# Kernel optimization log

Measured on AMD Instinct MI355X. Metric: run time of the kernel, lower is better.

Reference implementation:

```python
import jax, jax.numpy as jnp
import numpy as np

N = 1_048_576   # number of input points
C = 64          # feature channels
GRID = 128      # voxels per spatial dim
BATCH = 4


def setup_inputs() -> dict:
    key = jax.random.key(0)
    k1, k2, k3 = jax.random.split(key, 3)
    # coords layout per scn: [x, y, z, batch_idx]
    xyz = jax.random.randint(k1, (N, 3), 0, GRID, dtype=jnp.int64)
    b = jax.random.randint(k2, (N, 1), 0, BATCH, dtype=jnp.int64)
    coords = jnp.concatenate([xyz, b], axis=1)
    features = jax.random.normal(k3, (N, C), dtype=jnp.float32)
    spatial_size = jnp.array([GRID, GRID, GRID], dtype=jnp.int64)
    return {"coords": coords, "features": features,
            "spatial_size": spatial_size, "batch_size": BATCH}


def reference(coords, features, spatial_size, batch_size):
    # Hash each (batch, x, y, z) coordinate to a unique linear voxel id,
    # then scatter-SUM (scn mode=3) features of duplicate coordinates.
    n = coords.shape[0]
    # row-major strides over spatial dims: [S1*S2, S2, 1]
    strides = jnp.concatenate([
        jnp.cumprod(spatial_size[::-1])[::-1][1:], jnp.ones((1,), jnp.int64)])
    vol = jnp.prod(spatial_size)
    lin = coords[:, -1] * vol + coords[:, :-1] @ strides  # [N] voxel ids

    # Unique active sites (padded to fixed size N for jit) + inverse map.
    uniq_ids, inv = jnp.unique(lin, size=n, fill_value=-1, return_inverse=True)
    inv = inv.reshape(n)

    # Scatter-reduce features into active sites (mode 3 = sum duplicates).
    sparse_features = jax.ops.segment_sum(features, inv, num_segments=n)
    return uniq_ids, sparse_features
```

## Files before the change

### kernel.cpp

```cpp
#include <hip/hip_runtime.h>

constexpr int GRID_D = 128;
constexpr int BATCHN = 4;
constexpr int C = 64;
constexpr int VOL = GRID_D * GRID_D * GRID_D;
constexpr int V = BATCHN * VOL;
constexpr int W = V / 32;
constexpr int SCAN_BS = 1024;
constexpr int SCAN_NB = W / SCAN_BS;

typedef float floatx4 __attribute__((ext_vector_type(4)));


__global__ void zero_ws(uint4* __restrict__ p, int count) {
    int i = blockIdx.x * blockDim.x + threadIdx.x;
    if (i < count) p[i] = uint4{0u, 0u, 0u, 0u};
}

__global__ void mark_bits(const int* __restrict__ coords, unsigned* __restrict__ bm,
                          unsigned* __restrict__ lin, int n) {
    int i = blockIdx.x * blockDim.x + threadIdx.x;
    if (i >= n) return;
    int4 co = reinterpret_cast<const int4*>(coords)[i];
    unsigned l = (unsigned)(co.w * VOL + co.x * (GRID_D * GRID_D) + co.y * GRID_D + co.z);
    lin[i] = l;
    atomicOr(&bm[l >> 5], 1u << (l & 31));
}

__global__ void scan1(const unsigned* __restrict__ bm, unsigned* __restrict__ wp,
                      unsigned* __restrict__ bs) {
    int idx = blockIdx.x * SCAN_BS + threadIdx.x;
    unsigned pc = __popc(bm[idx]);
    unsigned v = pc;
    #pragma unroll
    for (int d = 1; d < 64; d <<= 1) {
        unsigned t = __shfl_up(v, d, 64);
        if ((threadIdx.x & 63) >= d) v += t;
    }
    __shared__ unsigned wsum[16];
    int wid = threadIdx.x >> 6;
    int lane = threadIdx.x & 63;
    if (lane == 63) wsum[wid] = v;
    __syncthreads();
    if (threadIdx.x < 16) {
        unsigned s = wsum[threadIdx.x];
        #pragma unroll
        for (int d = 1; d < 16; d <<= 1) {
            unsigned t = __shfl_up(s, d, 16);
            if ((threadIdx.x & 15) >= d) s += t;
        }
        wsum[threadIdx.x] = s;
    }
    __syncthreads();
    unsigned waveoff = (wid == 0) ? 0u : wsum[wid - 1];
    wp[idx] = waveoff + v - pc;
    if (threadIdx.x == SCAN_BS - 1) bs[blockIdx.x] = waveoff + v;
}

__global__ void scan2(unsigned* bs) {
    int t = threadIdx.x;
    unsigned pc = bs[t];
    unsigned v = pc;
    #pragma unroll
    for (int d = 1; d < 64; d <<= 1) {
        unsigned tt = __shfl_up(v, d, 64);
        if ((t & 63) >= d) v += tt;
    }
    __shared__ unsigned wsum[4];
    int wid = t >> 6, lane = t & 63;
    if (lane == 63) wsum[wid] = v;
    __syncthreads();
    if (t < 4) {
        unsigned s = wsum[t];
        #pragma unroll
        for (int d = 1; d < 4; d <<= 1) {
            unsigned tt = __shfl_up(s, d, 4);
            if ((t & 3) >= d) s += tt;
        }
        wsum[t] = s;
    }
    __syncthreads();
    unsigned waveoff = (wid == 0) ? 0u : wsum[wid - 1];
    bs[t] = waveoff + v - pc;
    if (t == SCAN_NB - 1) bs[SCAN_NB] = waveoff + v;
}

__global__ void emit_uniq(const unsigned* __restrict__ bm, const unsigned* __restrict__ wp,
                          const unsigned* __restrict__ bs, float* __restrict__ out) {
    int idx = blockIdx.x * blockDim.x + threadIdx.x;
    unsigned word = bm[idx];
    unsigned base = wp[idx] + bs[idx >> 10];
    while (word) {
        int b = __ffs(word) - 1;
        out[base++] = (float)((idx << 5) + b);
        word &= word - 1;
    }
}

__global__ void rank_slot(const unsigned* __restrict__ lin, const unsigned* __restrict__ bm,
                          const unsigned* __restrict__ wp, const unsigned* __restrict__ bs,
                          unsigned* __restrict__ cnt, unsigned* __restrict__ slot0,
                          unsigned* __restrict__ slot1, uint2* __restrict__ ovf,
                          unsigned* __restrict__ ovfCnt, int n) {
    int i = blockIdx.x * blockDim.x + threadIdx.x;
    if (i >= n) return;
    unsigned l = lin[i];
    unsigned w = l >> 5, b = l & 31;
    unsigned rank = wp[w] + bs[w >> 10] + __popc(bm[w] & ((1u << b) - 1u));
    unsigned old = atomicAdd(&cnt[rank], 1u);
    if (old == 0) slot0[rank] = (unsigned)i;
    else if (old == 1) slot1[rank] = (unsigned)i;
    else {
        unsigned o = atomicAdd(ovfCnt, 1u);
        ovf[o] = uint2{rank, (unsigned)i};
    }
}

__global__ void gather_feat(const floatx4* __restrict__ feat4, const unsigned* __restrict__ cnt,
                            const unsigned* __restrict__ slot0, const unsigned* __restrict__ slot1,
                            float* __restrict__ out_ids, float* __restrict__ outf, int n) {
    int gid = blockIdx.x * blockDim.x + threadIdx.x;
    int rank = gid >> 4;
    int c4 = gid & 15;
    if (rank >= n) return;
    unsigned c = cnt[rank];
    floatx4 v = {0.f, 0.f, 0.f, 0.f};
    if (c >= 1) {
        unsigned p0 = slot0[rank];
        v = __builtin_nontemporal_load(&feat4[(size_t)p0 * 16 + c4]);
        if (c >= 2) {
            unsigned p1 = slot1[rank];
            floatx4 u = __builtin_nontemporal_load(&feat4[(size_t)p1 * 16 + c4]);
            v.x += u.x; v.y += u.y; v.z += u.z; v.w += u.w;
        }
    } else if (c4 == 0) {
        out_ids[rank] = -1.0f;
    }
    __builtin_nontemporal_store(v, reinterpret_cast<floatx4*>(outf + (size_t)rank * C + c4 * 4));
}

__global__ void ovf_apply(const uint2* __restrict__ ovf, const unsigned* __restrict__ ovfCnt,
                          const floatx4* __restrict__ feat4, float* __restrict__ outf) {
    unsigned m = *ovfCnt;
    unsigned stride = gridDim.x * blockDim.x;
    for (unsigned idx = blockIdx.x * blockDim.x + threadIdx.x; idx < m * 16; idx += stride) {
        unsigned e = idx >> 4, c4 = idx & 15;
        uint2 rp = ovf[e];
        floatx4 v = feat4[(size_t)rp.y * 16 + c4];
        float* dst = outf + (size_t)rp.x * C + c4 * 4;
        atomicAdd(dst + 0, v.x);
        atomicAdd(dst + 1, v.y);
        atomicAdd(dst + 2, v.z);
        atomicAdd(dst + 3, v.w);
    }
}


extern "C" void kernel_launch(void* const* d_in, const int* in_sizes, int n_in,
                              void* d_out, int out_size, void* d_ws, size_t ws_size,
                              hipStream_t stream) {
    const int* coords = (const int*)d_in[0];
    const float* feat = (const float*)d_in[1];
    int n = in_sizes[0] / 4;

    float* out_ids = (float*)d_out;
    float* out_feat = (float*)d_out + n;

    unsigned* cnt = (unsigned*)d_ws;
    unsigned* ovfCnt = cnt + n;
    unsigned* bm = ovfCnt + 64;
    unsigned* wp = bm + W;
    unsigned* bs = wp + W;
    unsigned* lin = bs + SCAN_NB + 64;
    unsigned* slot0 = lin + n;
    unsigned* slot1 = slot0 + n;
    uint2* ovf = (uint2*)(slot1 + n);

    int zero_words = n + 64 + W;
    int zero_u4 = zero_words / 4;
    zero_ws<<<(zero_u4 + 255) / 256, 256, 0, stream>>>((uint4*)d_ws, zero_u4);

    mark_bits<<<(n + 255) / 256, 256, 0, stream>>>(coords, bm, lin, n);
    scan1<<<SCAN_NB, SCAN_BS, 0, stream>>>(bm, wp, bs);
    scan2<<<1, SCAN_NB, 0, stream>>>(bs);
    emit_uniq<<<W / 256, 256, 0, stream>>>(bm, wp, bs, out_ids);
    rank_slot<<<(n + 255) / 256, 256, 0, stream>>>(lin, bm, wp, bs, cnt, slot0, slot1,
                                                   ovf, ovfCnt, n);
    gather_feat<<<(n * 16) / 256, 256, 0, stream>>>((const floatx4*)feat, cnt, slot0, slot1,
                                                    out_ids, out_feat, n);
    ovf_apply<<<128, 256, 0, stream>>>(ovf, ovfCnt, (const floatx4*)feat, out_feat);
}
```

Baseline: 235.0 us.

## Pack per-voxel count and slot indices into one uint4 metadata record

Replaces the separate cnt, slot0 and slot1 arrays with an interleaved 16-byte record per unique voxel, so gather_feat reads all metadata with a single vector load. gather_feat also becomes a grid-stride loop over a fixed 16384-block grid, and its feature loads switch from nontemporal to regular loads. The cost is that zeroing now covers four words per point instead of one, roughly quadrupling that memset. rank_slot's atomics and stores now land on a strided layout.

```diff
diff --git a/kernel.cpp b/kernel.cpp
--- a/kernel.cpp
+++ b/kernel.cpp
@@ -99,44 +99,42 @@
 
 __global__ void rank_slot(const unsigned* __restrict__ lin, const unsigned* __restrict__ bm,
                           const unsigned* __restrict__ wp, const unsigned* __restrict__ bs,
-                          unsigned* __restrict__ cnt, unsigned* __restrict__ slot0,
-                          unsigned* __restrict__ slot1, uint2* __restrict__ ovf,
+                          unsigned* __restrict__ metau, uint2* __restrict__ ovf,
                           unsigned* __restrict__ ovfCnt, int n) {
     int i = blockIdx.x * blockDim.x + threadIdx.x;
     if (i >= n) return;
     unsigned l = lin[i];
     unsigned w = l >> 5, b = l & 31;
     unsigned rank = wp[w] + bs[w >> 10] + __popc(bm[w] & ((1u << b) - 1u));
-    unsigned old = atomicAdd(&cnt[rank], 1u);
-    if (old == 0) slot0[rank] = (unsigned)i;
-    else if (old == 1) slot1[rank] = (unsigned)i;
+    unsigned old = atomicAdd(&metau[rank * 4], 1u);
+    if (old == 0) metau[rank * 4 + 1] = (unsigned)i;
+    else if (old == 1) metau[rank * 4 + 2] = (unsigned)i;
     else {
         unsigned o = atomicAdd(ovfCnt, 1u);
         ovf[o] = uint2{rank, (unsigned)i};
     }
 }
 
-__global__ void gather_feat(const floatx4* __restrict__ feat4, const unsigned* __restrict__ cnt,
-                            const unsigned* __restrict__ slot0, const unsigned* __restrict__ slot1,
+__global__ void gather_feat(const floatx4* __restrict__ feat4, const uint4* __restrict__ meta,
                             float* __restrict__ out_ids, float* __restrict__ outf, int n) {
-    int gid = blockIdx.x * blockDim.x + threadIdx.x;
-    int rank = gid >> 4;
-    int c4 = gid & 15;
-    if (rank >= n) return;
-    unsigned c = cnt[rank];
-    floatx4 v = {0.f, 0.f, 0.f, 0.f};
-    if (c >= 1) {
-        unsigned p0 = slot0[rank];
-        v = __builtin_nontemporal_load(&feat4[(size_t)p0 * 16 + c4]);
-        if (c >= 2) {
-            unsigned p1 = slot1[rank];
-            floatx4 u = __builtin_nontemporal_load(&feat4[(size_t)p1 * 16 + c4]);
-            v.x += u.x; v.y += u.y; v.z += u.z; v.w += u.w;
+    int stride = gridDim.x * blockDim.x;
+    int total = n * 16;
+    for (int gid = blockIdx.x * blockDim.x + threadIdx.x; gid < total; gid += stride) {
+        int rank = gid >> 4;
+        int c4 = gid & 15;
+        uint4 m = meta[rank];
+        floatx4 v = {0.f, 0.f, 0.f, 0.f};
+        if (m.x >= 1) {
+            v = feat4[(size_t)m.y * 16 + c4];
+            if (m.x >= 2) {
+                floatx4 u = feat4[(size_t)m.z * 16 + c4];
+                v += u;
+            }
+        } else if (c4 == 0) {
+            out_ids[rank] = -1.0f;
         }
-    } else if (c4 == 0) {
-        out_ids[rank] = -1.0f;
+        __builtin_nontemporal_store(v, reinterpret_cast<floatx4*>(outf + (size_t)rank * C + c4 * 4));
     }
-    __builtin_nontemporal_store(v, reinterpret_cast<floatx4*>(outf + (size_t)rank * C + c4 * 4));
 }
 
 __global__ void ovf_apply(const uint2* __restrict__ ovf, const unsigned* __restrict__ ovfCnt,
@@ -166,27 +164,24 @@
     float* out_ids = (float*)d_out;
     float* out_feat = (float*)d_out + n;
 
-    unsigned* cnt = (unsigned*)d_ws;
-    unsigned* ovfCnt = cnt + n;
+    unsigned* metau = (unsigned*)d_ws;
+    unsigned* ovfCnt = metau + 4 * (size_t)n;
     unsigned* bm = ovfCnt + 64;
     unsigned* wp = bm + W;
     unsigned* bs = wp + W;
     unsigned* lin = bs + SCAN_NB + 64;
-    unsigned* slot0 = lin + n;
-    unsigned* slot1 = slot0 + n;
-    uint2* ovf = (uint2*)(slot1 + n);
+    uint2* ovf = (uint2*)(lin + n);
 
-    int zero_words = n + 64 + W;
-    int zero_u4 = zero_words / 4;
+    size_t zero_words = 4 * (size_t)n + 64 + W;
+    int zero_u4 = (int)(zero_words / 4);
     zero_ws<<<(zero_u4 + 255) / 256, 256, 0, stream>>>((uint4*)d_ws, zero_u4);
 
     mark_bits<<<(n + 255) / 256, 256, 0, stream>>>(coords, bm, lin, n);
     scan1<<<SCAN_NB, SCAN_BS, 0, stream>>>(bm, wp, bs);
     scan2<<<1, SCAN_NB, 0, stream>>>(bs);
     emit_uniq<<<W / 256, 256, 0, stream>>>(bm, wp, bs, out_ids);
-    rank_slot<<<(n + 255) / 256, 256, 0, stream>>>(lin, bm, wp, bs, cnt, slot0, slot1,
-                                                   ovf, ovfCnt, n);
-    gather_feat<<<(n * 16) / 256, 256, 0, stream>>>((const floatx4*)feat, cnt, slot0, slot1,
-                                                    out_ids, out_feat, n);
+    rank_slot<<<(n + 255) / 256, 256, 0, stream>>>(lin, bm, wp, bs, metau, ovf, ovfCnt, n);
+    gather_feat<<<16384, 256, 0, stream>>>((const floatx4*)feat, (const uint4*)metau,
+                                           out_ids, out_feat, n);
     ovf_apply<<<128, 256, 0, stream>>>(ovf, ovfCnt, (const floatx4*)feat, out_feat);
 }
```

Result: no change. 231.3 us (-1.6%).
